# Performance work log

Measured on AMD Instinct MI355X. Metric: run time of the kernel, lower is better.

## Reference

```python
import jax, jax.numpy as jnp
import numpy as np

B, T, D = 4, 2048, 256   # batch, temporal_scale, input_dim
H = 8                    # num_heads (hard-coded in module)
DH = D // H              # head dim
DFF = 512                # dim_feedforward (hard-coded)
WIN = 9                  # window_size
EPS = 1e-5               # LayerNorm eps


def _window_mask(t, h, w):
    # True = masked (disallowed). Each row j allows columns clip(j - w//2 + k, 0, t-1), k in [0, w).
    rows = jnp.arange(t)[:, None]                                   # [t,1]
    cols = jnp.clip(rows - w // 2 + jnp.arange(w)[None, :], 0, t - 1)  # [t,w]
    allowed = jnp.zeros((t, t), dtype=bool).at[rows, cols].set(True)
    # local_len == num_heads == 8: every head gets the same window mask
    return jnp.broadcast_to(~allowed, (h, t, t))                    # [H,T,T]


def setup_inputs() -> dict:
    key = jax.random.key(0)
    ks = jax.random.split(key, 6)
    s = 0.05
    return {
        "features": jax.random.normal(ks[0], (B, T, D), jnp.float32),
        "w_qkv": jax.random.normal(ks[1], (3 * D, D), jnp.float32) * s,
        "b_qkv": jnp.zeros((3 * D,), jnp.float32),
        "w_out": jax.random.normal(ks[2], (D, D), jnp.float32) * s,
        "b_out": jnp.zeros((D,), jnp.float32),
        "w1": jax.random.normal(ks[3], (DFF, D), jnp.float32) * s,
        "b1": jnp.zeros((DFF,), jnp.float32),
        "w2": jax.random.normal(ks[4], (D, DFF), jnp.float32) * s,
        "b2": jnp.zeros((D,), jnp.float32),
        "g1": jnp.ones((D,), jnp.float32),
        "be1": jnp.zeros((D,), jnp.float32),
        "g2": jnp.ones((D,), jnp.float32),
        "be2": jnp.zeros((D,), jnp.float32),
        "mask": _window_mask(T, H, WIN),
    }


def _layernorm(x, g, b):
    mu = jnp.mean(x, axis=-1, keepdims=True)
    var = jnp.var(x, axis=-1, keepdims=True)
    return (x - mu) * jax.lax.rsqrt(var + EPS) * g + b


def reference(features, w_qkv, b_qkv, w_out, b_out, w1, b1, w2, b2,
              g1, be1, g2, be2, mask):
    b, t, d = features.shape
    # --- windowed multi-head self-attention (dropout = eval-mode identity) ---
    qkv = features @ w_qkv.T + b_qkv                         # [b,t,3d]
    q, k, v = jnp.split(qkv, 3, axis=-1)
    split_heads = lambda x: x.reshape(b, t, H, DH).transpose(0, 2, 1, 3)  # [b,H,t,dh]
    q, k, v = split_heads(q), split_heads(k), split_heads(v)
    scores = jnp.einsum('bhqd,bhkd->bhqk', q, k) / jnp.sqrt(jnp.float32(DH))
    scores = jnp.where(mask[None], -jnp.inf, scores)         # mask True = disallowed
    attn = jax.nn.softmax(scores, axis=-1)                   # [b,H,t,t]
    o = jnp.einsum('bhqk,bhkd->bhqd', attn, v)
    o = o.transpose(0, 2, 1, 3).reshape(b, t, d)
    o = o @ w_out.T + b_out
    # --- residual + norm1 ---
    x = _layernorm(features + o, g1, be1)
    # --- FFN (relu) + residual + norm2 ---
    ff = jax.nn.relu(x @ w1.T + b1) @ w2.T + b2
    return _layernorm(x + ff, g2, be2)
```

## Files before the change

### kernel.cpp

```cpp
#include <hip/hip_runtime.h>
#include <math.h>

#define T_LEN 2048
#define LN_EPS 1e-5f
#define M_ROWS 8192

using u16x8  = __attribute__((ext_vector_type(8))) unsigned short;
using bf16x8 = __attribute__((ext_vector_type(8))) short;
using f32x4  = __attribute__((ext_vector_type(4))) float;

__device__ __forceinline__ unsigned short f2bf(float f) {
    unsigned int u = __float_as_uint(f);
    u += 0x7FFFu + ((u >> 16) & 1u);
    return (unsigned short)(u >> 16);
}
__device__ __forceinline__ float bf2f(unsigned short u) {
    return __uint_as_float(((unsigned int)u) << 16);
}
__device__ __forceinline__ u16x8 pack8(float4 a, float4 c) {
    u16x8 p;
    p[0] = f2bf(a.x); p[1] = f2bf(a.y); p[2] = f2bf(a.z); p[3] = f2bf(a.w);
    p[4] = f2bf(c.x); p[5] = f2bf(c.y); p[6] = f2bf(c.z); p[7] = f2bf(c.w);
    return p;
}
__device__ __forceinline__ void gload16(const void* g, void* l) {
    __builtin_amdgcn_global_load_lds(
        (const __attribute__((address_space(1))) unsigned int*)g,
        (__attribute__((address_space(3))) unsigned int*)l, 16, 0, 0);
}
__device__ __forceinline__ void bar_vm4() {
    asm volatile("s_waitcnt vmcnt(4)" ::: "memory");
    __builtin_amdgcn_s_barrier();
}
__device__ __forceinline__ void bar_vm0() {
    asm volatile("s_waitcnt vmcnt(0)" ::: "memory");
    __builtin_amdgcn_s_barrier();
}

__global__ __launch_bounds__(512) void qkv_gemm_f32(
    const float* __restrict__ A, const float* __restrict__ W,
    const float* __restrict__ bias,
    const float* __restrict__ wo, const float* __restrict__ w1,
    const float* __restrict__ w2,
    unsigned short* __restrict__ C, unsigned short* __restrict__ wconv)
{
    __shared__ char sm[2][40960];

    const int tid = threadIdx.x, lane = tid & 63, wid = tid >> 6;
    const int wr = wid >> 2, wcl = wid & 3;
    const int m0 = blockIdx.x * 128, n0 = blockIdx.y * 192;

    {
        const int bid = blockIdx.y * 64 + blockIdx.x;
        const int g = bid * 512 + tid;
        if (g < 40960) {
            const int e = g * 8;
            const float* src; int off;
            if (e < 65536)       { src = wo; off = 0; }
            else if (e < 196608) { src = w1; off = 65536; }
            else                 { src = w2; off = 196608; }
            const float4 a = *(const float4*)(src + (e - off));
            const float4 c = *(const float4*)(src + (e - off) + 4);
            *(u16x8*)(wconv + e) = pack8(a, c);
        }
    }

    float4 ld[5][2];
    auto LOADR = [&](int k0) {
        #pragma unroll
        for (int j = 0; j < 5; ++j) {
            const int i = j * 512 + tid;
            const float* src;
            if (i < 1024) {
                const int row = i >> 3, k8 = i & 7;
                src = A + (size_t)(m0 + row) * 256 + k0 + k8 * 8;
            } else {
                const int ii = i - 1024;
                const int row = ii >> 3, k8 = ii & 7;
                src = W + (size_t)(n0 + row) * 256 + k0 + k8 * 8;
            }
            ld[j][0] = *(const float4*)src;
            ld[j][1] = *(const float4*)(src + 4);
        }
    };
    auto CWRITE = [&](char* buf) {
        #pragma unroll
        for (int j = 0; j < 5; ++j) {
            const int i = j * 512 + tid;
            const u16x8 p = pack8(ld[j][0], ld[j][1]);
            if (i < 1024) {
                const int row = i >> 3, k8 = i & 7;
                *(u16x8*)(buf + ((row * 128 + k8 * 16) ^ ((row & 7) << 4))) = p;
            } else {
                const int ii = i - 1024;
                const int row = ii >> 3, k8 = ii & 7;
                *(u16x8*)(buf + 16384 + ((row * 128 + k8 * 16) ^ ((row & 7) << 4))) = p;
            }
        }
    };

    f32x4 acc[4][3];
    #pragma unroll
    for (int m = 0; m < 4; ++m)
        #pragma unroll
        for (int n = 0; n < 3; ++n) acc[m][n] = (f32x4)(0.f);

    LOADR(0);
    CWRITE(sm[0]);
    __syncthreads();

    #pragma unroll
    for (int k = 0; k < 4; ++k) {
        if (k < 3) LOADR((k + 1) * 64);
        char* As = sm[k & 1];
        char* Bs = sm[k & 1] + 16384;
        #pragma unroll
        for (int ks = 0; ks < 2; ++ks) {
            bf16x8 af[4], bfr[3];
            #pragma unroll
            for (int m = 0; m < 4; ++m) {
                const int row = wr * 64 + m * 16 + (lane & 15);
                const int off = (row * 128 + ks * 64 + (lane >> 4) * 16) ^ ((row & 7) << 4);
                af[m] = *(const bf16x8*)(As + off);
            }
            #pragma unroll
            for (int n = 0; n < 3; ++n) {
                const int row = wcl * 48 + n * 16 + (lane & 15);
                const int off = (row * 128 + ks * 64 + (lane >> 4) * 16) ^ ((row & 7) << 4);
                bfr[n] = *(const bf16x8*)(Bs + off);
            }
            #pragma unroll
            for (int m = 0; m < 4; ++m)
                #pragma unroll
                for (int n = 0; n < 3; ++n)
                    acc[m][n] = __builtin_amdgcn_mfma_f32_16x16x32_bf16(
                        af[m], bfr[n], acc[m][n], 0, 0, 0);
        }
        if (k < 3) CWRITE(sm[(k + 1) & 1]);
        __syncthreads();
    }

    #pragma unroll
    for (int n = 0; n < 3; ++n) {
        const int c = n0 + wcl * 48 + n * 16 + (lane & 15);
        const float bv = bias[c];
        #pragma unroll
        for (int m = 0; m < 4; ++m) {
            const int rbase = m0 + wr * 64 + m * 16 + ((lane >> 4) << 2);
            #pragma unroll
            for (int j = 0; j < 4; ++j)
                C[(size_t)(rbase + j) * 768 + c] = f2bf(acc[m][n][j] + bv);
        }
    }
}

__global__ __launch_bounds__(512) void tail_fused_pipe(
    const unsigned short* __restrict__ qkv, const unsigned short* __restrict__ Wo,
    const unsigned short* __restrict__ W1, const unsigned short* __restrict__ W2,
    const float* __restrict__ resf, const float* __restrict__ b_out,
    const float* __restrict__ g1, const float* __restrict__ be1,
    const float* __restrict__ b1, const float* __restrict__ b2,
    const float* __restrict__ g2, const float* __restrict__ be2,
    float* __restrict__ out)
{
    __shared__ __align__(16) char sm[149504];
    char* smA = sm;
    char* smH = sm + 114688;
    float* part = (float*)(sm + 147456);

    const int tid = threadIdx.x, lane = tid & 63, wid = tid >> 6;
    const int m0 = blockIdx.x * 32;
    const int b = m0 >> 11, t0 = m0 & 2047;

    auto stbuf = [&](int i) -> char* { return sm + 16384 + (i % 3) * 32768; };
    auto NSTAGE = [&](int i) {
        if (i >= 20) return;
        const unsigned short* W; int ldk, ro, k0;
        if (i < 4)       { W = Wo; ldk = 256; ro = 0;                    k0 = i * 64; }
        else if (i < 12) { W = W1; ldk = 256; ro = ((i - 4) >> 2) * 256; k0 = ((i - 4) & 3) * 64; }
        else             { W = W2; ldk = 512; ro = 0;                    k0 = (i - 12) * 64; }
        char* dst = stbuf(i);
        #pragma unroll
        for (int j = 0; j < 4; ++j) {
            const int ii = j * 512 + tid, row = ii >> 3, k8 = (ii & 7) ^ (row & 7);
            gload16(W + (size_t)(ro + row) * ldk + k0 + k8 * 8, dst + ii * 16);
        }
    };

    NSTAGE(0); NSTAGE(1);

    {
        const int half = tid & 1, p = tid >> 1;
        const int h = p & 7, tl = p >> 3;
        const int t = t0 + tl;
        const unsigned short* base = qkv + (size_t)b * T_LEN * 768;

        float q[16];
        const unsigned short* qp = base + (size_t)t * 768 + h * 32 + half * 16;
        #pragma unroll
        for (int jj = 0; jj < 2; ++jj) {
            u16x8 u = *(const u16x8*)(qp + jj * 8);
            #pragma unroll
            for (int e = 0; e < 8; ++e) q[jj * 8 + e] = bf2f(u[e]);
        }
        const unsigned short* kbase = base + 256 + h * 32 + half * 16;
        const unsigned short* vbase = base + 512 + h * 32 + half * 16;

        float sc[9], mx = -1e30f;
        #pragma unroll
        for (int j = 0; j < 9; ++j) {
            const int kr0 = t - 4 + j;
            const int krm = min(max(kr0, 0), T_LEN - 1);
            const unsigned short* kr = kbase + (size_t)krm * 768;
            float d = 0.f;
            #pragma unroll
            for (int jj = 0; jj < 2; ++jj) {
                u16x8 u = *(const u16x8*)(kr + jj * 8);
                #pragma unroll
                for (int e = 0; e < 8; ++e) d += q[jj * 8 + e] * bf2f(u[e]);
            }
            d += __shfl_xor(d, 1);
            sc[j] = (kr0 == krm) ? d * 0.17677669529663687f : -1e30f;
            mx = fmaxf(mx, sc[j]);
        }
        float sum = 0.f;
        #pragma unroll
        for (int j = 0; j < 9; ++j) { sc[j] = expf(sc[j] - mx); sum += sc[j]; }
        const float inv = 1.f / sum;

        float ov[16] = {};
        #pragma unroll
        for (int j = 0; j < 9; ++j) {
            const float pj = sc[j] * inv;
            const int krm = min(max(t - 4 + j, 0), T_LEN - 1);
            const unsigned short* vr = vbase + (size_t)krm * 768;
            #pragma unroll
            for (int jj = 0; jj < 2; ++jj) {
                u16x8 u = *(const u16x8*)(vr + jj * 8);
                #pragma unroll
                for (int e = 0; e < 8; ++e) ov[jj * 8 + e] += pj * bf2f(u[e]);
            }
        }
        #pragma unroll
        for (int jj = 0; jj < 2; ++jj) {
            u16x8 p8;
            #pragma unroll
            for (int e = 0; e < 8; ++e) p8[e] = f2bf(ov[jj * 8 + e]);
            const int ch = h * 4 + half * 2 + jj;
            *(u16x8*)(smA + tl * 512 + ((ch ^ (tl & 7)) << 4)) = p8;
        }
    }
    __syncthreads();

    float xres[2][2][4];

    {
        f32x4 acc[2][2];
        #pragma unroll
        for (int m = 0; m < 2; ++m)
            #pragma unroll
            for (int n = 0; n < 2; ++n) acc[m][n] = (f32x4)(0.f);

        #pragma unroll
        for (int i = 0; i < 4; ++i) {
            NSTAGE(i + 2);
            char* Bs = stbuf(i);
            #pragma unroll
            for (int ks = 0; ks < 2; ++ks) {
                bf16x8 af[2], bfr[2];
                #pragma unroll
                for (int m = 0; m < 2; ++m) {
                    const int r = m * 16 + (lane & 15);
                    const int ch = i * 8 + ks * 4 + (lane >> 4);
                    af[m] = *(const bf16x8*)(smA + r * 512 + ((ch ^ (r & 7)) << 4));
                }
                #pragma unroll
                for (int n = 0; n < 2; ++n) {
                    const int rB = wid * 32 + n * 16 + (lane & 15);
                    bfr[n] = *(const bf16x8*)(Bs + rB * 128
                             + (((ks * 4 + (lane >> 4)) ^ (rB & 7)) << 4));
                }
                #pragma unroll
                for (int m = 0; m < 2; ++m)
                    #pragma unroll
                    for (int n = 0; n < 2; ++n)
                        acc[m][n] = __builtin_amdgcn_mfma_f32_16x16x32_bf16(
                            af[m], bfr[n], acc[m][n], 0, 0, 0);
            }
            bar_vm4();
        }

        float v[2][2][4], s[2][4], sq[2][4];
        #pragma unroll
        for (int m = 0; m < 2; ++m)
            #pragma unroll
            for (int j = 0; j < 4; ++j) { s[m][j] = 0.f; sq[m][j] = 0.f; }
        #pragma unroll
        for (int n = 0; n < 2; ++n) {
            const int c = wid * 32 + n * 16 + (lane & 15);
            const float bv = b_out[c];
            #pragma unroll
            for (int m = 0; m < 2; ++m) {
                const int rb = m * 16 + ((lane >> 4) << 2);
                #pragma unroll
                for (int j = 0; j < 4; ++j) {
                    float x = acc[m][n][j] + bv + resf[(size_t)(m0 + rb + j) * 256 + c];
                    v[m][n][j] = x; s[m][j] += x; sq[m][j] += x * x;
                }
            }
        }
        #pragma unroll
        for (int m = 0; m < 2; ++m)
            #pragma unroll
            for (int j = 0; j < 4; ++j) {
                #pragma unroll
                for (int msk = 1; msk <= 8; msk <<= 1) {
                    s[m][j]  += __shfl_xor(s[m][j], msk);
                    sq[m][j] += __shfl_xor(sq[m][j], msk);
                }
                if ((lane & 15) == 0) {
                    const int r = m * 16 + ((lane >> 4) << 2) + j;
                    part[(wid * 32 + r) * 2 + 0] = s[m][j];
                    part[(wid * 32 + r) * 2 + 1] = sq[m][j];
                }
            }
        __syncthreads();
        #pragma unroll
        for (int m = 0; m < 2; ++m) {
            const int rb = m * 16 + ((lane >> 4) << 2);
            #pragma unroll
            for (int j = 0; j < 4; ++j) {
                const int r = rb + j;
                float S = 0.f, SQ = 0.f;
                #pragma unroll
                for (int w = 0; w < 8; ++w) {
                    S += part[(w * 32 + r) * 2 + 0]; SQ += part[(w * 32 + r) * 2 + 1];
                }
                const float mean = S * (1.f / 256.f);
                const float var  = SQ * (1.f / 256.f) - mean * mean;
                const float rstd = rsqrtf(var + LN_EPS);
                #pragma unroll
                for (int n = 0; n < 2; ++n) {
                    const int c = wid * 32 + n * 16 + (lane & 15);
                    const float o = (v[m][n][j] - mean) * rstd * g1[c] + be1[c];
                    xres[m][n][j] = o;
                    const int addr = r * 512 + (((c >> 3) ^ (r & 7)) << 4) + ((c & 7) << 1);
                    *(unsigned short*)(smA + addr) = f2bf(o);
                }
            }
        }
    }
    __syncthreads();

    {
        f32x4 acc[2][2];
        #pragma unroll
        for (int m = 0; m < 2; ++m)
            #pragma unroll
            for (int n = 0; n < 2; ++n) acc[m][n] = (f32x4)(0.f);

        #pragma unroll
        for (int i = 4; i < 12; ++i) {
            NSTAGE(i + 2);
            const int kk = (i - 4) & 3, half = (i - 4) >> 2;
            char* Bs = stbuf(i);
            #pragma unroll
            for (int ks = 0; ks < 2; ++ks) {
                bf16x8 af[2], bfr[2];
                #pragma unroll
                for (int m = 0; m < 2; ++m) {
                    const int r = m * 16 + (lane & 15);
                    const int ch = kk * 8 + ks * 4 + (lane >> 4);
                    af[m] = *(const bf16x8*)(smA + r * 512 + ((ch ^ (r & 7)) << 4));
                }
                #pragma unroll
                for (int n = 0; n < 2; ++n) {
                    const int rB = wid * 32 + n * 16 + (lane & 15);
                    bfr[n] = *(const bf16x8*)(Bs + rB * 128
                             + (((ks * 4 + (lane >> 4)) ^ (rB & 7)) << 4));
                }
                #pragma unroll
                for (int m = 0; m < 2; ++m)
                    #pragma unroll
                    for (int n = 0; n < 2; ++n)
                        acc[m][n] = __builtin_amdgcn_mfma_f32_16x16x32_bf16(
                            af[m], bfr[n], acc[m][n], 0, 0, 0);
            }
            bar_vm4();
            if (kk == 3) {
                #pragma unroll
                for (int n = 0; n < 2; ++n) {
                    const int c = half * 256 + wid * 32 + n * 16 + (lane & 15);
                    const float bv = b1[c];
                    #pragma unroll
                    for (int m = 0; m < 2; ++m) {
                        const int rb = m * 16 + ((lane >> 4) << 2);
                        #pragma unroll
                        for (int j = 0; j < 4; ++j) {
                            const int rr = rb + j;
                            const int addr = rr * 1024 + (((c >> 3) ^ (rr & 7)) << 4)
                                           + ((c & 7) << 1);
                            *(unsigned short*)(smH + addr) =
                                f2bf(fmaxf(acc[m][n][j] + bv, 0.f));
                        }
                    }
                }
                #pragma unroll
                for (int m = 0; m < 2; ++m)
                    #pragma unroll
                    for (int n = 0; n < 2; ++n) acc[m][n] = (f32x4)(0.f);
            }
        }
    }
    __syncthreads();

    {
        f32x4 acc[2][2];
        #pragma unroll
        for (int m = 0; m < 2; ++m)
            #pragma unroll
            for (int n = 0; n < 2; ++n) acc[m][n] = (f32x4)(0.f);

        #pragma unroll
        for (int i = 12; i < 20; ++i) {
            NSTAGE(i + 2);
            const int k = i - 12;
            char* Bs = stbuf(i);
            #pragma unroll
            for (int ks = 0; ks < 2; ++ks) {
                bf16x8 af[2], bfr[2];
                #pragma unroll
                for (int m = 0; m < 2; ++m) {
                    const int r = m * 16 + (lane & 15);
                    const int ch = k * 8 + ks * 4 + (lane >> 4);
                    af[m] = *(const bf16x8*)(smH + r * 1024 + ((ch ^ (r & 7)) << 4));
                }
                #pragma unroll
                for (int n = 0; n < 2; ++n) {
                    const int rB = wid * 32 + n * 16 + (lane & 15);
                    bfr[n] = *(const bf16x8*)(Bs + rB * 128
                             + (((ks * 4 + (lane >> 4)) ^ (rB & 7)) << 4));
                }
                #pragma unroll
                for (int m = 0; m < 2; ++m)
                    #pragma unroll
                    for (int n = 0; n < 2; ++n)
                        acc[m][n] = __builtin_amdgcn_mfma_f32_16x16x32_bf16(
                            af[m], bfr[n], acc[m][n], 0, 0, 0);
            }
            if (i + 2 < 20) bar_vm4(); else bar_vm0();
        }

        float v[2][2][4], s[2][4], sq[2][4];
        #pragma unroll
        for (int m = 0; m < 2; ++m)
            #pragma unroll
            for (int j = 0; j < 4; ++j) { s[m][j] = 0.f; sq[m][j] = 0.f; }
        #pragma unroll
        for (int n = 0; n < 2; ++n) {
            const int c = wid * 32 + n * 16 + (lane & 15);
            const float bv = b2[c];
            #pragma unroll
            for (int m = 0; m < 2; ++m) {
                #pragma unroll
                for (int j = 0; j < 4; ++j) {
                    float x = acc[m][n][j] + bv + xres[m][n][j];
                    v[m][n][j] = x; s[m][j] += x; sq[m][j] += x * x;
                }
            }
        }
        #pragma unroll
        for (int m = 0; m < 2; ++m)
            #pragma unroll
            for (int j = 0; j < 4; ++j) {
                #pragma unroll
                for (int msk = 1; msk <= 8; msk <<= 1) {
                    s[m][j]  += __shfl_xor(s[m][j], msk);
                    sq[m][j] += __shfl_xor(sq[m][j], msk);
                }
                if ((lane & 15) == 0) {
                    const int r = m * 16 + ((lane >> 4) << 2) + j;
                    part[(wid * 32 + r) * 2 + 0] = s[m][j];
                    part[(wid * 32 + r) * 2 + 1] = sq[m][j];
                }
            }
        __syncthreads();
        #pragma unroll
        for (int m = 0; m < 2; ++m) {
            const int rb = m * 16 + ((lane >> 4) << 2);
            #pragma unroll
            for (int j = 0; j < 4; ++j) {
                const int r = rb + j;
                float S = 0.f, SQ = 0.f;
                #pragma unroll
                for (int w = 0; w < 8; ++w) {
                    S += part[(w * 32 + r) * 2 + 0]; SQ += part[(w * 32 + r) * 2 + 1];
                }
                const float mean = S * (1.f / 256.f);
                const float var  = SQ * (1.f / 256.f) - mean * mean;
                const float rstd = rsqrtf(var + LN_EPS);
                #pragma unroll
                for (int n = 0; n < 2; ++n) {
                    const int c = wid * 32 + n * 16 + (lane & 15);
                    out[(size_t)(m0 + r) * 256 + c] =
                        (v[m][n][j] - mean) * rstd * g2[c] + be2[c];
                }
            }
        }
    }
}

extern "C" void kernel_launch(void* const* d_in, const int* in_sizes, int n_in,
                              void* d_out, int out_size, void* d_ws, size_t ws_size,
                              hipStream_t stream) {
    const float* features = (const float*)d_in[0];
    const float* w_qkv    = (const float*)d_in[1];
    const float* b_qkv    = (const float*)d_in[2];
    const float* w_out    = (const float*)d_in[3];
    const float* b_out    = (const float*)d_in[4];
    const float* w1       = (const float*)d_in[5];
    const float* b1       = (const float*)d_in[6];
    const float* w2       = (const float*)d_in[7];
    const float* b2       = (const float*)d_in[8];
    const float* g1       = (const float*)d_in[9];
    const float* be1      = (const float*)d_in[10];
    const float* g2       = (const float*)d_in[11];
    const float* be2      = (const float*)d_in[12];

    unsigned short* wsu = (unsigned short*)d_ws;
    unsigned short* wconv = wsu;
    unsigned short* qkvbf = wsu + 327680;
    unsigned short* wobf  = wconv;
    unsigned short* w1bf  = wconv + 65536;
    unsigned short* w2bf  = wconv + 196608;

    qkv_gemm_f32<<<dim3(64, 4), 512, 0, stream>>>(
        features, w_qkv, b_qkv, w_out, w1, w2, qkvbf, wconv);
    tail_fused_pipe<<<M_ROWS / 32, 512, 0, stream>>>(
        qkvbf, wobf, w1bf, w2bf, features, b_out, g1, be1, b1, b2, g2, be2,
        (float*)d_out);
}
```

Measured before the change: 37.69 us.

## Move Q projection into fused tail kernel, compute only K/V in first GEMM

The first GEMM now produces only K and V (512 columns) and also converts W_q to bf16. The tail kernel computes Q for its 32-row tile from features with an extra MFMA stage over the pipelined weight buffers and keeps Q in shared memory. This cuts the first kernel's work and its Q writeback/readback through global memory. In exchange the tail kernel gets a longer pipeline with more barriers, and it reads features again.

```diff
diff --git a/kernel.cpp b/kernel.cpp
--- a/kernel.cpp
+++ b/kernel.cpp
@@ -37,38 +37,39 @@
     __builtin_amdgcn_s_barrier();
 }
 
-__global__ __launch_bounds__(512) void qkv_gemm_f32(
-    const float* __restrict__ A, const float* __restrict__ W,
+__global__ __launch_bounds__(512) void kv_gemm_f32(
+    const float* __restrict__ A, const float* __restrict__ Wqkv,
     const float* __restrict__ bias,
     const float* __restrict__ wo, const float* __restrict__ w1,
     const float* __restrict__ w2,
-    unsigned short* __restrict__ C, unsigned short* __restrict__ wconv)
+    unsigned short* __restrict__ KV, unsigned short* __restrict__ wconv)
 {
-    __shared__ char sm[2][40960];
+    __shared__ char sm[2][32768];
 
     const int tid = threadIdx.x, lane = tid & 63, wid = tid >> 6;
     const int wr = wid >> 2, wcl = wid & 3;
-    const int m0 = blockIdx.x * 128, n0 = blockIdx.y * 192;
+    const int m0 = blockIdx.x * 128, n0 = blockIdx.y * 128;
 
     {
         const int bid = blockIdx.y * 64 + blockIdx.x;
         const int g = bid * 512 + tid;
-        if (g < 40960) {
+        if (g < 49152) {
             const int e = g * 8;
             const float* src; int off;
-            if (e < 65536)       { src = wo; off = 0; }
-            else if (e < 196608) { src = w1; off = 65536; }
-            else                 { src = w2; off = 196608; }
+            if (e < 65536)       { src = Wqkv; off = 0; }
+            else if (e < 131072) { src = wo;   off = 65536; }
+            else if (e < 262144) { src = w1;   off = 131072; }
+            else                 { src = w2;   off = 262144; }
             const float4 a = *(const float4*)(src + (e - off));
             const float4 c = *(const float4*)(src + (e - off) + 4);
             *(u16x8*)(wconv + e) = pack8(a, c);
         }
     }
 
-    float4 ld[5][2];
+    float4 ld[4][2];
     auto LOADR = [&](int k0) {
         #pragma unroll
-        for (int j = 0; j < 5; ++j) {
+        for (int j = 0; j < 4; ++j) {
             const int i = j * 512 + tid;
             const float* src;
             if (i < 1024) {
@@ -77,7 +78,7 @@
             } else {
                 const int ii = i - 1024;
                 const int row = ii >> 3, k8 = ii & 7;
-                src = W + (size_t)(n0 + row) * 256 + k0 + k8 * 8;
+                src = Wqkv + (size_t)(256 + n0 + row) * 256 + k0 + k8 * 8;
             }
             ld[j][0] = *(const float4*)src;
             ld[j][1] = *(const float4*)(src + 4);
@@ -85,7 +86,7 @@
     };
     auto CWRITE = [&](char* buf) {
         #pragma unroll
-        for (int j = 0; j < 5; ++j) {
+        for (int j = 0; j < 4; ++j) {
             const int i = j * 512 + tid;
             const u16x8 p = pack8(ld[j][0], ld[j][1]);
             if (i < 1024) {
@@ -99,11 +100,11 @@
         }
     };
 
-    f32x4 acc[4][3];
+    f32x4 acc[4][2];
     #pragma unroll
     for (int m = 0; m < 4; ++m)
         #pragma unroll
-        for (int n = 0; n < 3; ++n) acc[m][n] = (f32x4)(0.f);
+        for (int n = 0; n < 2; ++n) acc[m][n] = (f32x4)(0.f);
 
     LOADR(0);
     CWRITE(sm[0]);
@@ -113,10 +114,10 @@
     for (int k = 0; k < 4; ++k) {
         if (k < 3) LOADR((k + 1) * 64);
         char* As = sm[k & 1];
-        char* Bs = sm[k & 1] + 16384;
+        char* Ws = sm[k & 1] + 16384;
         #pragma unroll
         for (int ks = 0; ks < 2; ++ks) {
-            bf16x8 af[4], bfr[3];
+            bf16x8 af[4], bfr[2];
             #pragma unroll
             for (int m = 0; m < 4; ++m) {
                 const int row = wr * 64 + m * 16 + (lane & 15);
@@ -124,15 +125,15 @@
                 af[m] = *(const bf16x8*)(As + off);
             }
             #pragma unroll
-            for (int n = 0; n < 3; ++n) {
-                const int row = wcl * 48 + n * 16 + (lane & 15);
+            for (int n = 0; n < 2; ++n) {
+                const int row = wcl * 32 + n * 16 + (lane & 15);
                 const int off = (row * 128 + ks * 64 + (lane >> 4) * 16) ^ ((row & 7) << 4);
-                bfr[n] = *(const bf16x8*)(Bs + off);
+                bfr[n] = *(const bf16x8*)(Ws + off);
             }
             #pragma unroll
             for (int m = 0; m < 4; ++m)
                 #pragma unroll
-                for (int n = 0; n < 3; ++n)
+                for (int n = 0; n < 2; ++n)
                     acc[m][n] = __builtin_amdgcn_mfma_f32_16x16x32_bf16(
                         af[m], bfr[n], acc[m][n], 0, 0, 0);
         }
@@ -141,23 +142,23 @@
     }
 
     #pragma unroll
-    for (int n = 0; n < 3; ++n) {
-        const int c = n0 + wcl * 48 + n * 16 + (lane & 15);
-        const float bv = bias[c];
+    for (int n = 0; n < 2; ++n) {
+        const int c = n0 + wcl * 32 + n * 16 + (lane & 15);
+        const float bv = bias[256 + c];
         #pragma unroll
         for (int m = 0; m < 4; ++m) {
             const int rbase = m0 + wr * 64 + m * 16 + ((lane >> 4) << 2);
             #pragma unroll
             for (int j = 0; j < 4; ++j)
-                C[(size_t)(rbase + j) * 768 + c] = f2bf(acc[m][n][j] + bv);
-        }
-    }
-}
-
-__global__ __launch_bounds__(512) void tail_fused_pipe(
-    const unsigned short* __restrict__ qkv, const unsigned short* __restrict__ Wo,
-    const unsigned short* __restrict__ W1, const unsigned short* __restrict__ W2,
-    const float* __restrict__ resf, const float* __restrict__ b_out,
+                KV[(size_t)(rbase + j) * 512 + c] = f2bf(acc[m][n][j] + bv);
+        }
+    }
+}
+
+__global__ __launch_bounds__(512) void tail_fused_pipe2(
+    const unsigned short* __restrict__ kv, const unsigned short* __restrict__ wconv,
+    const float* __restrict__ features, const float* __restrict__ b_qkv,
+    const float* __restrict__ b_out,
     const float* __restrict__ g1, const float* __restrict__ be1,
     const float* __restrict__ b1, const float* __restrict__ b2,
     const float* __restrict__ g2, const float* __restrict__ be2,
@@ -166,19 +167,27 @@
     __shared__ __align__(16) char sm[149504];
     char* smA = sm;
     char* smH = sm + 114688;
+    char* smF = smH;
+    char* smQ = smH + 16384;
     float* part = (float*)(sm + 147456);
 
     const int tid = threadIdx.x, lane = tid & 63, wid = tid >> 6;
     const int m0 = blockIdx.x * 32;
     const int b = m0 >> 11, t0 = m0 & 2047;
 
+    const unsigned short* Wq = wconv;
+    const unsigned short* Wo = wconv + 65536;
+    const unsigned short* W1 = wconv + 131072;
+    const unsigned short* W2 = wconv + 262144;
+
     auto stbuf = [&](int i) -> char* { return sm + 16384 + (i % 3) * 32768; };
     auto NSTAGE = [&](int i) {
-        if (i >= 20) return;
+        if (i >= 24) return;
         const unsigned short* W; int ldk, ro, k0;
-        if (i < 4)       { W = Wo; ldk = 256; ro = 0;                    k0 = i * 64; }
-        else if (i < 12) { W = W1; ldk = 256; ro = ((i - 4) >> 2) * 256; k0 = ((i - 4) & 3) * 64; }
-        else             { W = W2; ldk = 512; ro = 0;                    k0 = (i - 12) * 64; }
+        if (i < 4)       { W = Wq; ldk = 256; ro = 0;                    k0 = i * 64; }
+        else if (i < 8)  { W = Wo; ldk = 256; ro = 0;                    k0 = (i - 4) * 64; }
+        else if (i < 16) { W = W1; ldk = 256; ro = ((i - 8) >> 2) * 256; k0 = ((i - 8) & 3) * 64; }
+        else             { W = W2; ldk = 512; ro = 0;                    k0 = (i - 16) * 64; }
         char* dst = stbuf(i);
         #pragma unroll
         for (int j = 0; j < 4; ++j) {
@@ -189,70 +198,16 @@
 
     NSTAGE(0); NSTAGE(1);
 
-    {
-        const int half = tid & 1, p = tid >> 1;
-        const int h = p & 7, tl = p >> 3;
-        const int t = t0 + tl;
-        const unsigned short* base = qkv + (size_t)b * T_LEN * 768;
-
-        float q[16];
-        const unsigned short* qp = base + (size_t)t * 768 + h * 32 + half * 16;
-        #pragma unroll
-        for (int jj = 0; jj < 2; ++jj) {
-            u16x8 u = *(const u16x8*)(qp + jj * 8);
-            #pragma unroll
-            for (int e = 0; e < 8; ++e) q[jj * 8 + e] = bf2f(u[e]);
-        }
-        const unsigned short* kbase = base + 256 + h * 32 + half * 16;
-        const unsigned short* vbase = base + 512 + h * 32 + half * 16;
-
-        float sc[9], mx = -1e30f;
-        #pragma unroll
-        for (int j = 0; j < 9; ++j) {
-            const int kr0 = t - 4 + j;
-            const int krm = min(max(kr0, 0), T_LEN - 1);
-            const unsigned short* kr = kbase + (size_t)krm * 768;
-            float d = 0.f;
-            #pragma unroll
-            for (int jj = 0; jj < 2; ++jj) {
-                u16x8 u = *(const u16x8*)(kr + jj * 8);
-                #pragma unroll
-                for (int e = 0; e < 8; ++e) d += q[jj * 8 + e] * bf2f(u[e]);
-            }
-            d += __shfl_xor(d, 1);
-            sc[j] = (kr0 == krm) ? d * 0.17677669529663687f : -1e30f;
-            mx = fmaxf(mx, sc[j]);
-        }
-        float sum = 0.f;
-        #pragma unroll
-        for (int j = 0; j < 9; ++j) { sc[j] = expf(sc[j] - mx); sum += sc[j]; }
-        const float inv = 1.f / sum;
-
-        float ov[16] = {};
-        #pragma unroll
-        for (int j = 0; j < 9; ++j) {
-            const float pj = sc[j] * inv;
-            const int krm = min(max(t - 4 + j, 0), T_LEN - 1);
-            const unsigned short* vr = vbase + (size_t)krm * 768;
-            #pragma unroll
-            for (int jj = 0; jj < 2; ++jj) {
-                u16x8 u = *(const u16x8*)(vr + jj * 8);
-                #pragma unroll
-                for (int e = 0; e < 8; ++e) ov[jj * 8 + e] += pj * bf2f(u[e]);
-            }
-        }
-        #pragma unroll
-        for (int jj = 0; jj < 2; ++jj) {
-            u16x8 p8;
-            #pragma unroll
-            for (int e = 0; e < 8; ++e) p8[e] = f2bf(ov[jj * 8 + e]);
-            const int ch = h * 4 + half * 2 + jj;
-            *(u16x8*)(smA + tl * 512 + ((ch ^ (tl & 7)) << 4)) = p8;
-        }
+    #pragma unroll
+    for (int j = 0; j < 2; ++j) {
+        const int i = j * 512 + tid;
+        const int e = i >> 5, ch = i & 31;
+        const float* src = features + ((size_t)(b * T_LEN + t0 + e)) * 256 + ch * 8;
+        const float4 a = *(const float4*)src;
+        const float4 c = *(const float4*)(src + 4);
+        *(u16x8*)(smF + e * 512 + ((ch ^ (e & 7)) << 4)) = pack8(a, c);
     }
     __syncthreads();
-
-    float xres[2][2][4];
 
     {
         f32x4 acc[2][2];
@@ -272,7 +227,7 @@
                 for (int m = 0; m < 2; ++m) {
                     const int r = m * 16 + (lane & 15);
                     const int ch = i * 8 + ks * 4 + (lane >> 4);
-                    af[m] = *(const bf16x8*)(smA + r * 512 + ((ch ^ (r & 7)) << 4));
+                    af[m] = *(const bf16x8*)(smF + r * 512 + ((ch ^ (r & 7)) << 4));
                 }
                 #pragma unroll
                 for (int n = 0; n < 2; ++n) {
@@ -289,6 +244,125 @@
             }
             bar_vm4();
         }
+        #pragma unroll
+        for (int n = 0; n < 2; ++n) {
+            const int c = wid * 32 + n * 16 + (lane & 15);
+            const float bv = b_qkv[c];
+            #pragma unroll
+            for (int m = 0; m < 2; ++m) {
+                const int rb = m * 16 + ((lane >> 4) << 2);
+                #pragma unroll
+                for (int j = 0; j < 4; ++j) {
+                    const int r = rb + j;
+                    const int addr = r * 512 + (((c >> 3) ^ (r & 7)) << 4) + ((c & 7) << 1);
+                    *(unsigned short*)(smQ + addr) = f2bf(acc[m][n][j] + bv);
+                }
+            }
+        }
+    }
+    __syncthreads();
+
+    {
+        const int half = tid & 1, p = tid >> 1;
+        const int h = p & 7, tl = p >> 3;
+        const int t = t0 + tl;
+        const unsigned short* kvb = kv + (size_t)b * T_LEN * 512;
+
+        float q[16];
+        #pragma unroll
+        for (int jj = 0; jj < 2; ++jj) {
+            const int ch = h * 4 + half * 2 + jj;
+            u16x8 u = *(const u16x8*)(smQ + tl * 512 + ((ch ^ (tl & 7)) << 4));
+            #pragma unroll
+            for (int e = 0; e < 8; ++e) q[jj * 8 + e] = bf2f(u[e]);
+        }
+        const unsigned short* kbase = kvb + h * 32 + half * 16;
+        const unsigned short* vbase = kvb + 256 + h * 32 + half * 16;
+
+        float sc[9], mx = -1e30f;
+        #pragma unroll
+        for (int j = 0; j < 9; ++j) {
+            const int kr0 = t - 4 + j;
+            const int krm = min(max(kr0, 0), T_LEN - 1);
+            const unsigned short* kr = kbase + (size_t)krm * 512;
+            float d = 0.f;
+            #pragma unroll
+            for (int jj = 0; jj < 2; ++jj) {
+                u16x8 u = *(const u16x8*)(kr + jj * 8);
+                #pragma unroll
+                for (int e = 0; e < 8; ++e) d += q[jj * 8 + e] * bf2f(u[e]);
+            }
+            d += __shfl_xor(d, 1);
+            sc[j] = (kr0 == krm) ? d * 0.17677669529663687f : -1e30f;
+            mx = fmaxf(mx, sc[j]);
+        }
+        float sum = 0.f;
+        #pragma unroll
+        for (int j = 0; j < 9; ++j) { sc[j] = expf(sc[j] - mx); sum += sc[j]; }
+        const float inv = 1.f / sum;
+
+        float ov[16] = {};
+        #pragma unroll
+        for (int j = 0; j < 9; ++j) {
+            const float pj = sc[j] * inv;
+            const int krm = min(max(t - 4 + j, 0), T_LEN - 1);
+            const unsigned short* vr = vbase + (size_t)krm * 512;
+            #pragma unroll
+            for (int jj = 0; jj < 2; ++jj) {
+                u16x8 u = *(const u16x8*)(vr + jj * 8);
+                #pragma unroll
+                for (int e = 0; e < 8; ++e) ov[jj * 8 + e] += pj * bf2f(u[e]);
+            }
+        }
+        #pragma unroll
+        for (int jj = 0; jj < 2; ++jj) {
+            u16x8 p8;
+            #pragma unroll
+            for (int e = 0; e < 8; ++e) p8[e] = f2bf(ov[jj * 8 + e]);
+            const int ch = h * 4 + half * 2 + jj;
+            *(u16x8*)(smA + tl * 512 + ((ch ^ (tl & 7)) << 4)) = p8;
+        }
+    }
+    __syncthreads();
+
+    float xres[2][2][4];
+
+    {
+        f32x4 acc[2][2];
+        #pragma unroll
+        for (int m = 0; m < 2; ++m)
+            #pragma unroll
+            for (int n = 0; n < 2; ++n) acc[m][n] = (f32x4)(0.f);
+
+        #pragma unroll
+        for (int i = 4; i < 8; ++i) {
+            NSTAGE(i + 2);
+            const int kk = i - 4;
+            char* Bs = stbuf(i);
+            #pragma unroll
+            for (int ks = 0; ks < 2; ++ks) {
+                bf16x8 af[2], bfr[2];
+                #pragma unroll
+                for (int m = 0; m < 2; ++m) {
+                    const int r = m * 16 + (lane & 15);
+                    const int ch = kk * 8 + ks * 4 + (lane >> 4);
+                    af[m] = *(const bf16x8*)(smA + r * 512 + ((ch ^ (r & 7)) << 4));
+                }
+                #pragma unroll
+                for (int n = 0; n < 2; ++n) {
+                    const int rB = wid * 32 + n * 16 + (lane & 15);
+                    bfr[n] = *(const bf16x8*)(Bs + rB * 128
+                             + (((ks * 4 + (lane >> 4)) ^ (rB & 7)) << 4));
+                }
+                #pragma unroll
+                for (int m = 0; m < 2; ++m)
+                    #pragma unroll
+                    for (int n = 0; n < 2; ++n)
+                        acc[m][n] = __builtin_amdgcn_mfma_f32_16x16x32_bf16(
+                            af[m], bfr[n], acc[m][n], 0, 0, 0);
+            }
+            bar_vm4();
+        }
 
         float v[2][2][4], s[2][4], sq[2][4];
         #pragma unroll
@@ -304,7 +378,8 @@
                 const int rb = m * 16 + ((lane >> 4) << 2);
                 #pragma unroll
                 for (int j = 0; j < 4; ++j) {
-                    float x = acc[m][n][j] + bv + resf[(size_t)(m0 + rb + j) * 256 + c];
+                    float x = acc[m][n][j] + bv
+                            + features[(size_t)(m0 + rb + j) * 256 + c];
                     v[m][n][j] = x; s[m][j] += x; sq[m][j] += x * x;
                 }
             }
@@ -360,9 +435,9 @@
             for (int n = 0; n < 2; ++n) acc[m][n] = (f32x4)(0.f);
 
         #pragma unroll
-        for (int i = 4; i < 12; ++i) {
+        for (int i = 8; i < 16; ++i) {
             NSTAGE(i + 2);
-            const int kk = (i - 4) & 3, half = (i - 4) >> 2;
+            const int kk = (i - 8) & 3, half = (i - 8) >> 2;
             char* Bs = stbuf(i);
             #pragma unroll
             for (int ks = 0; ks < 2; ++ks) {
@@ -422,9 +497,9 @@
             for (int n = 0; n < 2; ++n) acc[m][n] = (f32x4)(0.f);
 
         #pragma unroll
-        for (int i = 12; i < 20; ++i) {
+        for (int i = 16; i < 24; ++i) {
             NSTAGE(i + 2);
-            const int k = i - 12;
+            const int k = i - 16;
             char* Bs = stbuf(i);
             #pragma unroll
             for (int ks = 0; ks < 2; ++ks) {
@@ -448,7 +523,7 @@
                         acc[m][n] = __builtin_amdgcn_mfma_f32_16x16x32_bf16(
                             af[m], bfr[n], acc[m][n], 0, 0, 0);
             }
-            if (i + 2 < 20) bar_vm4(); else bar_vm0();
+            if (i + 2 < 24) bar_vm4(); else bar_vm0();
         }
 
         float v[2][2][4], s[2][4], sq[2][4];
@@ -529,14 +604,11 @@
 
     unsigned short* wsu = (unsigned short*)d_ws;
     unsigned short* wconv = wsu;
-    unsigned short* qkvbf = wsu + 327680;
-    unsigned short* wobf  = wconv;
-    unsigned short* w1bf  = wconv + 65536;
-    unsigned short* w2bf  = wconv + 196608;
-
-    qkv_gemm_f32<<<dim3(64, 4), 512, 0, stream>>>(
-        features, w_qkv, b_qkv, w_out, w1, w2, qkvbf, wconv);
-    tail_fused_pipe<<<M_ROWS / 32, 512, 0, stream>>>(
-        qkvbf, wobf, w1bf, w2bf, features, b_out, g1, be1, b1, b2, g2, be2,
+    unsigned short* kvbf  = wsu + 393216;
+
+    kv_gemm_f32<<<dim3(64, 4), 512, 0, stream>>>(
+        features, w_qkv, b_qkv, w_out, w1, w2, kvbf, wconv);
+    tail_fused_pipe2<<<M_ROWS / 32, 512, 0, stream>>>(
+        kvbf, wconv, features, b_qkv, b_out, g1, be1, b1, b2, g2, be2,
         (float*)d_out);
 }
```

Measured after the change: 37.40 us, median of 2. About the same (-0.8%).
